# Optimization experiments

Measured on AMD Instinct MI355X. Metric: run time of the kernel, lower is better.

## Reference

```python
import jax, jax.numpy as jnp
import numpy as np

N_NODES = 100000
N_EDGES = 1600000
N_GRAPHS = 512
IN_DIM = 128
HID = 128
N_CLASSES = 10


def _gcn_conv(x, W, b, src, dst, n):
    """PyG GCNConv: out = D^{-1/2} (A+I) D^{-1/2} (x @ W) + b."""
    xw = x @ W  # [n, out_dim]
    loop = jnp.arange(n)
    s = jnp.concatenate([src, loop])  # add self loops
    d = jnp.concatenate([dst, loop])
    deg = jax.ops.segment_sum(jnp.ones(s.shape, dtype=xw.dtype), d, num_segments=n)
    dinv = jnp.where(deg > 0, jax.lax.rsqrt(deg), jnp.zeros((), xw.dtype))
    norm = dinv[s] * dinv[d]  # [E + n]
    out = jax.ops.segment_sum(xw[s] * norm[:, None], d, num_segments=n)
    return out + b


def _global_mean_pool(x, batch, num_graphs):
    sums = jax.ops.segment_sum(x, batch, num_segments=num_graphs)
    cnts = jax.ops.segment_sum(jnp.ones(batch.shape, dtype=x.dtype), batch, num_segments=num_graphs)
    return sums / jnp.maximum(cnts, 1.0)[:, None]


def setup_inputs() -> dict:
    key = jax.random.key(0)
    ks = jax.random.split(key, 8)
    x = jax.random.normal(ks[0], (N_NODES, IN_DIM), dtype=jnp.float32)
    edge_index = jax.random.randint(ks[1], (2, N_EDGES), 0, N_NODES, dtype=jnp.int64)
    batch = jnp.sort(jax.random.randint(ks[2], (N_NODES,), 0, N_GRAPHS, dtype=jnp.int64))
    sc = 1.0 / np.sqrt(IN_DIM)
    W1 = jax.random.normal(ks[3], (IN_DIM, HID), dtype=jnp.float32) * sc
    b1 = jnp.zeros((HID,), dtype=jnp.float32)
    W2 = jax.random.normal(ks[4], (HID, HID), dtype=jnp.float32) * (1.0 / np.sqrt(HID))
    b2 = jnp.zeros((HID,), dtype=jnp.float32)
    Wc = jax.random.normal(ks[5], (HID, N_CLASSES), dtype=jnp.float32) * (1.0 / np.sqrt(HID))
    bc = jnp.zeros((N_CLASSES,), dtype=jnp.float32)
    return {"x": x, "edge_index": edge_index, "batch": batch,
            "W1": W1, "b1": b1, "W2": W2, "b2": b2, "Wc": Wc, "bc": bc}


def reference(x, edge_index, batch, W1, b1, W2, b2, Wc, bc):
    src, dst = edge_index[0], edge_index[1]
    n = x.shape[0]
    h = _gcn_conv(x, W1, b1, src, dst, n)
    h = jax.nn.relu(h)
    h = _gcn_conv(h, W2, b2, src, dst, n)
    g = _global_mean_pool(h, batch, N_GRAPHS)
    return g @ Wc + bc
```

## Files before the change

### kernel.cpp

```cpp
#include <hip/hip_runtime.h>

#define N_NODES 100000
#define N_EDGES 1600000
#define N_GRAPHS 512
#define DIM 128
#define NCLS 10
#define NBKT 782
#define BCAP 2560

typedef __attribute__((ext_vector_type(8))) short short8;
typedef __attribute__((ext_vector_type(4))) float f32x4;

static __device__ __forceinline__ unsigned short f2bf(float f) {
    unsigned u = __float_as_uint(f);
    unsigned r = (u + 0x7FFF + ((u >> 16) & 1)) >> 16;
    return (unsigned short)r;
}
static __device__ __forceinline__ float bf2f(unsigned u) {
    return __uint_as_float(u << 16);
}


__global__ void k_wprep(const float* __restrict__ W1, const float* __restrict__ W2,
                        unsigned short* __restrict__ wf1, unsigned short* __restrict__ wf2,
                        int* __restrict__ bcnt, int* __restrict__ deg) {
    int b = blockIdx.x;
    if (b >= 128) {
        if (b < 132) {
            int i = (b - 128) * 256 + threadIdx.x;
            if (i < NBKT) bcnt[i] = 0;
        } else {
            int i = (b - 132) * 256 + threadIdx.x;
            if (i < N_NODES) deg[i] = 0;
        }
        return;
    }
    const float* W = (b < 64) ? W1 : W2;
    unsigned short* wfrag = (b < 64) ? wf1 : wf2;
    int t = (b & 63) * 256 + threadIdx.x;
    int j = t & 7, lane = (t >> 3) & 63, nt = (t >> 9) & 7, kit = t >> 12;
    int k = kit * 32 + (lane >> 4) * 8 + j;
    int n = nt * 16 + (lane & 15);
    float v = W[k * 128 + n];
    unsigned short h = f2bf(v);
    wfrag[t] = h;
    wfrag[16384 + t] = f2bf(v - bf2f(h));
}


__global__ __launch_bounds__(256) void k_bucket(
    const int* __restrict__ src, const int* __restrict__ dst,
    int* __restrict__ bcnt, unsigned* __restrict__ bpack,
    int* __restrict__ deg, int E) {
    __shared__ int cnt[NBKT];
    __shared__ int base[NBKT];
    int tid = threadIdx.x;
    for (int i = tid; i < NBKT; i += 256) cnt[i] = 0;
    __syncthreads();
    int e0 = blockIdx.x * 4096 + tid;
    unsigned pk[16]; short bk[16];
#pragma unroll
    for (int j = 0; j < 16; j++) {
        int e = e0 + j * 256;
        if (e < E) {
            int s = src[e], d = dst[e];
            atomicAdd(&deg[d], 1);
            bk[j] = (short)(d >> 7);
            pk[j] = ((unsigned)(d & 127) << 17) | (unsigned)s;
            atomicAdd(&cnt[bk[j]], 1);
        } else bk[j] = -1;
    }
    __syncthreads();
    for (int i = tid; i < NBKT; i += 256) {
        int c = cnt[i];
        base[i] = c ? atomicAdd(&bcnt[i], c) : 0;
        cnt[i] = 0;
    }
    __syncthreads();
#pragma unroll
    for (int j = 0; j < 16; j++) {
        if (bk[j] >= 0) {
            int p = base[bk[j]] + atomicAdd(&cnt[bk[j]], 1);
            if (p < BCAP) bpack[(size_t)bk[j] * BCAP + p] = pk[j];
        }
    }
}


static __device__ __forceinline__ void bsort_body(
    char* smemraw, int b,
    const unsigned* __restrict__ bpack, const int* __restrict__ bcnt,
    int* __restrict__ rp, float* __restrict__ dinv,
    int* __restrict__ esrc, int N) {
    int* lds      = (int*)smemraw;
    int* cnt      = lds + 256;
    int* scan     = lds + 384;
    int* cur      = lds + 512;
    int* gbase_sh = lds + 640;
    int tid = threadIdx.x;
    int v[4], pre[4];
    int s = 0;
#pragma unroll
    for (int j = 0; j < 4; j++) {
        int idx = tid * 4 + j;
        v[j] = (idx < NBKT) ? min(bcnt[idx], BCAP) : 0;
        pre[j] = s; s += v[j];
    }
    lds[tid] = s;
    __syncthreads();
    for (int off = 1; off < 256; off <<= 1) {
        int t = (tid >= off) ? lds[tid - off] : 0;
        __syncthreads();
        lds[tid] += t;
        __syncthreads();
    }
    if (tid == (b >> 2)) *gbase_sh = lds[tid] - s + pre[b & 3];
    if (tid < 128) cnt[tid] = 0;
    __syncthreads();
    int gbase = *gbase_sh;
    int n0 = b << 7;
    int m = min(bcnt[b], BCAP);
    const unsigned* bp = bpack + (size_t)b * BCAP;
    for (int j = tid; j < m; j += 256) atomicAdd(&cnt[bp[j] >> 17], 1);
    __syncthreads();
    if (tid < 128) scan[tid] = cnt[tid];
    __syncthreads();
    for (int off = 1; off < 128; off <<= 1) {
        int t = (tid < 128 && tid >= off) ? scan[tid - off] : 0;
        __syncthreads();
        if (tid < 128) scan[tid] += t;
        __syncthreads();
    }
    if (tid < 128) {
        int c = cnt[tid];
        int excl = scan[tid] - c;
        int node = n0 + tid;
        if (node <= N) rp[node] = gbase + excl;
        if (node < N) dinv[node] = rsqrtf((float)(c + 1));
        cur[tid] = gbase + excl;
    }
    __syncthreads();
    for (int j = tid; j < m; j += 256) {
        unsigned pk = bp[j];
        int p = atomicAdd(&cur[pk >> 17], 1);
        esrc[p] = (int)(pk & 0x1FFFF);
    }
}

static __device__ __forceinline__ void gemm_f32_body(
    char* smemraw, int rowBlk,
    const float* __restrict__ A, const unsigned short* __restrict__ wfrag,
    const int* __restrict__ deg, unsigned short* __restrict__ ybf, int M) {
    unsigned short* ldsw = (unsigned short*)smemraw;
    int tid = threadIdx.x, wave = tid >> 6, lane = tid & 63;
    int m = lane & 15, quad = lane >> 4;
    int rowBase = rowBlk * 128 + wave * 32;
    int r0 = rowBase + m, r1 = rowBase + 16 + m;
    for (int i = tid; i < 2048; i += 256)
        ((short8*)ldsw)[i] = ((const short8*)wfrag)[i];
    __syncthreads();
    f32x4 acc0[8], acc1[8];
#pragma unroll
    for (int i = 0; i < 8; i++) { acc0[i] = (f32x4){0,0,0,0}; acc1[i] = (f32x4){0,0,0,0}; }
    const unsigned short* wlo = wfrag + 16384;

#pragma unroll
    for (int kit = 0; kit < 4; kit++) {
        float a0[8], a1[8];
        if (r0 < M) {
            const float4* ap = (const float4*)(A + (size_t)r0 * 128 + kit * 32 + quad * 8);
            float4 f0 = ap[0], f1 = ap[1];
            a0[0]=f0.x; a0[1]=f0.y; a0[2]=f0.z; a0[3]=f0.w; a0[4]=f1.x; a0[5]=f1.y; a0[6]=f1.z; a0[7]=f1.w;
        } else { for (int j = 0; j < 8; j++) a0[j] = 0.f; }
        if (r1 < M) {
            const float4* ap = (const float4*)(A + (size_t)r1 * 128 + kit * 32 + quad * 8);
            float4 f0 = ap[0], f1 = ap[1];
            a1[0]=f0.x; a1[1]=f0.y; a1[2]=f0.z; a1[3]=f0.w; a1[4]=f1.x; a1[5]=f1.y; a1[6]=f1.z; a1[7]=f1.w;
        } else { for (int j = 0; j < 8; j++) a1[j] = 0.f; }
        short8 ahi0, alo0, ahi1, alo1;
#pragma unroll
        for (int j = 0; j < 8; j++) {
            unsigned short h0 = f2bf(a0[j]);
            ahi0[j] = (short)h0; alo0[j] = (short)f2bf(a0[j] - bf2f(h0));
            unsigned short h1 = f2bf(a1[j]);
            ahi1[j] = (short)h1; alo1[j] = (short)f2bf(a1[j] - bf2f(h1));
        }
        int fb = kit * 4096 + lane * 8;
#pragma unroll
        for (int nt = 0; nt < 8; nt++) {
            int idx = fb + nt * 512;
            short8 bhi = *(const short8*)(ldsw + idx);
            short8 blo = *(const short8*)(wlo + idx);
            acc0[nt] = __builtin_amdgcn_mfma_f32_16x16x32_bf16(ahi0, bhi, acc0[nt], 0, 0, 0);
            acc0[nt] = __builtin_amdgcn_mfma_f32_16x16x32_bf16(alo0, bhi, acc0[nt], 0, 0, 0);
            acc0[nt] = __builtin_amdgcn_mfma_f32_16x16x32_bf16(ahi0, blo, acc0[nt], 0, 0, 0);
            acc1[nt] = __builtin_amdgcn_mfma_f32_16x16x32_bf16(ahi1, bhi, acc1[nt], 0, 0, 0);
            acc1[nt] = __builtin_amdgcn_mfma_f32_16x16x32_bf16(alo1, bhi, acc1[nt], 0, 0, 0);
            acc1[nt] = __builtin_amdgcn_mfma_f32_16x16x32_bf16(ahi1, blo, acc1[nt], 0, 0, 0);
        }
    }
    __syncthreads();
    float dv0 = (r0 < M) ? rsqrtf((float)deg[r0] + 1.0f) : 0.f;
    float dv1 = (r1 < M) ? rsqrtf((float)deg[r1] + 1.0f) : 0.f;
    unsigned short* wsm = ldsw + wave * 32 * 136;
#pragma unroll
    for (int rg = 0; rg < 4; rg++) {
        float s0 = __shfl(dv0, quad * 4 + rg);
        float s1 = __shfl(dv1, quad * 4 + rg);
#pragma unroll
        for (int nt = 0; nt < 8; nt++) {
            wsm[(quad * 4 + rg) * 136 + nt * 16 + m] = f2bf(acc0[nt][rg] * s0);
            wsm[(16 + quad * 4 + rg) * 136 + nt * 16 + m] = f2bf(acc1[nt][rg] * s1);
        }
    }
    __syncthreads();
#pragma unroll
    for (int i = 0; i < 8; i++) {
        int rl = i * 4 + quad;
        int grow = rowBase + rl;
        if (grow < M) {
            short8 v = *(const short8*)(wsm + rl * 136 + m * 8);
            *(short8*)(ybf + (size_t)grow * 128 + m * 8) = v;
        }
    }
}


__global__ __launch_bounds__(256) void k_p3(
    const unsigned* __restrict__ bpack, const int* __restrict__ bcnt,
    int* __restrict__ rp, float* __restrict__ dinv, int* __restrict__ esrc, int N,
    const float* __restrict__ A, const unsigned short* __restrict__ wfrag,
    const int* __restrict__ deg, unsigned short* __restrict__ ybf, int M) {
    __shared__ __align__(16) char smem[4 * 32 * 136 * 2];
    if ((int)blockIdx.x < NBKT) bsort_body(smem, blockIdx.x, bpack, bcnt, rp, dinv, esrc, N);
    else                        gemm_f32_body(smem, blockIdx.x - NBKT, A, wfrag, deg, ybf, M);
}


__global__ __launch_bounds__(256) void k_gemm_bf(
    const unsigned short* __restrict__ A, const unsigned short* __restrict__ wfrag,
    const float* __restrict__ dinv, unsigned short* __restrict__ ybf, int M) {
    __shared__ unsigned short ldsw[4 * 32 * 136];
    int tid = threadIdx.x, wave = tid >> 6, lane = tid & 63;
    int m = lane & 15, quad = lane >> 4;
    int rowBase = blockIdx.x * 128 + wave * 32;
    int r0 = rowBase + m, r1 = rowBase + 16 + m;
    for (int i = tid; i < 2048; i += 256)
        ((short8*)ldsw)[i] = ((const short8*)wfrag)[i];
    __syncthreads();
    f32x4 acc0[8], acc1[8];
#pragma unroll
    for (int i = 0; i < 8; i++) { acc0[i] = (f32x4){0,0,0,0}; acc1[i] = (f32x4){0,0,0,0}; }
    const unsigned short* wlo = wfrag + 16384;

#pragma unroll
    for (int kit = 0; kit < 4; kit++) {
        short8 ah0, ah1;
        if (r0 < M) ah0 = *(const short8*)(A + (size_t)r0 * 128 + kit * 32 + quad * 8);
        else { for (int j = 0; j < 8; j++) ah0[j] = 0; }
        if (r1 < M) ah1 = *(const short8*)(A + (size_t)r1 * 128 + kit * 32 + quad * 8);
        else { for (int j = 0; j < 8; j++) ah1[j] = 0; }
        int fb = kit * 4096 + lane * 8;
#pragma unroll
        for (int nt = 0; nt < 8; nt++) {
            int idx = fb + nt * 512;
            short8 bhi = *(const short8*)(ldsw + idx);
            short8 blo = *(const short8*)(wlo + idx);
            acc0[nt] = __builtin_amdgcn_mfma_f32_16x16x32_bf16(ah0, bhi, acc0[nt], 0, 0, 0);
            acc0[nt] = __builtin_amdgcn_mfma_f32_16x16x32_bf16(ah0, blo, acc0[nt], 0, 0, 0);
            acc1[nt] = __builtin_amdgcn_mfma_f32_16x16x32_bf16(ah1, bhi, acc1[nt], 0, 0, 0);
            acc1[nt] = __builtin_amdgcn_mfma_f32_16x16x32_bf16(ah1, blo, acc1[nt], 0, 0, 0);
        }
    }
    __syncthreads();
    float dv0 = (r0 < M) ? dinv[r0] : 0.f;
    float dv1 = (r1 < M) ? dinv[r1] : 0.f;
    unsigned short* wsm = ldsw + wave * 32 * 136;
#pragma unroll
    for (int rg = 0; rg < 4; rg++) {
        float s0 = __shfl(dv0, quad * 4 + rg);
        float s1 = __shfl(dv1, quad * 4 + rg);
#pragma unroll
        for (int nt = 0; nt < 8; nt++) {
            wsm[(quad * 4 + rg) * 136 + nt * 16 + m] = f2bf(acc0[nt][rg] * s0);
            wsm[(16 + quad * 4 + rg) * 136 + nt * 16 + m] = f2bf(acc1[nt][rg] * s1);
        }
    }
    __syncthreads();
#pragma unroll
    for (int i = 0; i < 8; i++) {
        int rl = i * 4 + quad;
        int grow = rowBase + rl;
        if (grow < M) {
            short8 v = *(const short8*)(wsm + rl * 136 + m * 8);
            *(short8*)(ybf + (size_t)grow * 128 + m * 8) = v;
        }
    }
}


__global__ __launch_bounds__(256) void k_agg(
    const unsigned short* __restrict__ y, const float* __restrict__ dinv,
    const int* __restrict__ rp, const int* __restrict__ esrc,
    const float* __restrict__ bias, unsigned* __restrict__ out, int relu, int N) {
    int wave = threadIdx.x >> 6;
    int lane = threadIdx.x & 63;
    int node = blockIdx.x * 4 + wave;
    if (node >= N) return;
    const unsigned* y2 = (const unsigned*)y;
    unsigned vs = y2[(size_t)node * 64 + lane];
    float a0 = bf2f(vs & 0xFFFF), a1 = bf2f(vs >> 16);
    int beg = rp[node], end = rp[node + 1];
    int j = beg;
    while (j < end) {
        int idxv = (j + lane < end) ? esrc[j + lane] : 0;
        int cnt = end - j; if (cnt > 64) cnt = 64;
        int i = 0;
        for (; i + 4 <= cnt; i += 4) {
            int s0 = __shfl(idxv, i + 0);
            int s1 = __shfl(idxv, i + 1);
            int s2 = __shfl(idxv, i + 2);
            int s3 = __shfl(idxv, i + 3);
            unsigned v0 = y2[(size_t)s0 * 64 + lane];
            unsigned v1 = y2[(size_t)s1 * 64 + lane];
            unsigned v2 = y2[(size_t)s2 * 64 + lane];
            unsigned v3 = y2[(size_t)s3 * 64 + lane];
            a0 += bf2f(v0 & 0xFFFF); a1 += bf2f(v0 >> 16);
            a0 += bf2f(v1 & 0xFFFF); a1 += bf2f(v1 >> 16);
            a0 += bf2f(v2 & 0xFFFF); a1 += bf2f(v2 >> 16);
            a0 += bf2f(v3 & 0xFFFF); a1 += bf2f(v3 >> 16);
        }
        for (; i < cnt; i++) {
            int s = __shfl(idxv, i);
            unsigned v = y2[(size_t)s * 64 + lane];
            a0 += bf2f(v & 0xFFFF); a1 += bf2f(v >> 16);
        }
        j += cnt;
    }
    float s = dinv[node];
    float2 bv = ((const float2*)bias)[lane];
    float o0 = s * a0 + bv.x;
    float o1 = s * a1 + bv.y;
    if (relu) { o0 = fmaxf(o0, 0.f); o1 = fmaxf(o1, 0.f); }
    out[(size_t)node * 64 + lane] = (unsigned)f2bf(o0) | ((unsigned)f2bf(o1) << 16);
}


__global__ __launch_bounds__(256) void k_poolhead(
    const unsigned* __restrict__ h2, const int* __restrict__ batch,
    const float* __restrict__ Wc, const float* __restrict__ bc,
    float* __restrict__ out, int n) {
    __shared__ float2 red[4][64];
    __shared__ float grow[DIM];
    int gid = blockIdx.x;
    int tid = threadIdx.x, wave = tid >> 6, lane = tid & 63;
    int lo = 0, hi = n;
    while (lo < hi) { int mid = (lo + hi) >> 1; if (batch[mid] < gid) lo = mid + 1; else hi = mid; }
    int start = lo;
    hi = n;
    while (lo < hi) { int mid = (lo + hi) >> 1; if (batch[mid] < gid + 1) lo = mid + 1; else hi = mid; }
    int end = lo;
    float a0 = 0.f, a1 = 0.f;
    for (int r = start + wave; r < end; r += 4) {
        unsigned v = h2[(size_t)r * 64 + lane];
        a0 += bf2f(v & 0xFFFF); a1 += bf2f(v >> 16);
    }
    red[wave][lane] = make_float2(a0, a1);
    __syncthreads();
    if (tid < 64) {
        float2 s = red[0][tid];
        s.x += red[1][tid].x; s.y += red[1][tid].y;
        s.x += red[2][tid].x; s.y += red[2][tid].y;
        s.x += red[3][tid].x; s.y += red[3][tid].y;
        int cnt = end - start;
        float inv = 1.f / (float)(cnt > 0 ? cnt : 1);
        grow[tid * 2] = s.x * inv;
        grow[tid * 2 + 1] = s.y * inv;
    }
    __syncthreads();
    if (tid < NCLS) {
        float acc = bc[tid];
#pragma unroll 16
        for (int k = 0; k < DIM; k++) acc += grow[k] * Wc[k * NCLS + tid];
        out[gid * NCLS + tid] = acc;
    }
}

extern "C" void kernel_launch(void* const* d_in, const int* in_sizes, int n_in,
                              void* d_out, int out_size, void* d_ws, size_t ws_size,
                              hipStream_t stream) {
    const float* x    = (const float*)d_in[0];
    const int*   ei   = (const int*)d_in[1];
    const int*   batch= (const int*)d_in[2];
    const float* W1   = (const float*)d_in[3];
    const float* b1   = (const float*)d_in[4];
    const float* W2   = (const float*)d_in[5];
    const float* b2   = (const float*)d_in[6];
    const float* Wc   = (const float*)d_in[7];
    const float* bc   = (const float*)d_in[8];
    float* out = (float*)d_out;
    const int N = N_NODES, E = N_EDGES;
    const int* src = ei;
    const int* dst = ei + E;

    char* ws = (char*)d_ws;
    size_t off = 0;
    auto carve = [&](size_t bytes) -> void* {
        void* p = ws + off;
        off = (off + bytes + 255) & ~(size_t)255;
        return p;
    };
    int*      rp    = (int*)     carve((size_t)(N + 1) * 4);
    float*    dinv  = (float*)   carve((size_t)N * 4);
    int*      bcnt  = (int*)     carve(NBKT * 4);
    int*      deg   = (int*)     carve((size_t)N * 4);
    unsigned* bpack = (unsigned*)carve((size_t)NBKT * BCAP * 4);
    int*      esrc  = (int*)     carve((size_t)E * 4);
    unsigned short* wf1 = (unsigned short*)carve(2 * 16384 * 2);
    unsigned short* wf2 = (unsigned short*)carve(2 * 16384 * 2);
    unsigned short* bufY = (unsigned short*)carve((size_t)N * DIM * 2);
    unsigned short* bufH = (unsigned short*)carve((size_t)N * DIM * 2);
    (void)ws_size; (void)n_in; (void)in_sizes; (void)out_size;

    const int nbBkt = (E + 4095) / 4096;
    const int gemmGrid = (N + 127) / 128;
    const int degZero = (N + 255) / 256;

    hipLaunchKernelGGL(k_wprep, dim3(132 + degZero), dim3(256), 0, stream, W1, W2, wf1, wf2, bcnt, deg);
    hipLaunchKernelGGL(k_bucket, dim3(nbBkt), dim3(256), 0, stream, src, dst, bcnt, bpack, deg, E);
    hipLaunchKernelGGL(k_p3, dim3(NBKT + gemmGrid), dim3(256), 0, stream,
                       bpack, bcnt, rp, dinv, esrc, N, x, wf1, deg, bufY, N);
    hipLaunchKernelGGL(k_agg, dim3((N + 3) / 4), dim3(256), 0, stream, bufY, dinv, rp, esrc, b1, (unsigned*)bufH, 1, N);
    hipLaunchKernelGGL(k_gemm_bf, dim3(gemmGrid), dim3(256), 0, stream, bufH, wf2, dinv, bufY, N);
    hipLaunchKernelGGL(k_agg, dim3((N + 3) / 4), dim3(256), 0, stream, bufY, dinv, rp, esrc, b2, (unsigned*)bufH, 0, N);
    hipLaunchKernelGGL(k_poolhead, dim3(N_GRAPHS), dim3(256), 0, stream, (const unsigned*)bufH, batch, Wc, bc, out, N);
}
```

Baseline: 386.4 us.

## Fuse bucket sort with first GEMM per block and drop global degree atomics

Removes the global per-edge degree atomics and the deg array. Degrees now come from the per-bucket counts computed during the bucket sort. Each block of the merged kernel sorts one 128-node bucket, keeps the normalisation factors in shared memory, then runs the first-layer GEMM for the same 128 rows. This drops 1.6M global atomics and the zeroing pass, but the sort and GEMM phases within a block now run in sequence, no longer as separate concurrent blocks.

```diff
diff --git a/kernel.cpp b/kernel.cpp
--- a/kernel.cpp
+++ b/kernel.cpp
@@ -23,16 +23,11 @@
 
 __global__ void k_wprep(const float* __restrict__ W1, const float* __restrict__ W2,
                         unsigned short* __restrict__ wf1, unsigned short* __restrict__ wf2,
-                        int* __restrict__ bcnt, int* __restrict__ deg) {
+                        int* __restrict__ bcnt) {
     int b = blockIdx.x;
     if (b >= 128) {
-        if (b < 132) {
-            int i = (b - 128) * 256 + threadIdx.x;
-            if (i < NBKT) bcnt[i] = 0;
-        } else {
-            int i = (b - 132) * 256 + threadIdx.x;
-            if (i < N_NODES) deg[i] = 0;
-        }
+        int i = (b - 128) * 256 + threadIdx.x;
+        if (i < NBKT) bcnt[i] = 0;
         return;
     }
     const float* W = (b < 64) ? W1 : W2;
@@ -50,8 +45,7 @@
 
 __global__ __launch_bounds__(256) void k_bucket(
     const int* __restrict__ src, const int* __restrict__ dst,
-    int* __restrict__ bcnt, unsigned* __restrict__ bpack,
-    int* __restrict__ deg, int E) {
+    int* __restrict__ bcnt, unsigned* __restrict__ bpack, int E) {
     __shared__ int cnt[NBKT];
     __shared__ int base[NBKT];
     int tid = threadIdx.x;
@@ -64,7 +58,6 @@
         int e = e0 + j * 256;
         if (e < E) {
             int s = src[e], d = dst[e];
-            atomicAdd(&deg[d], 1);
             bk[j] = (short)(d >> 7);
             pk[j] = ((unsigned)(d & 127) << 17) | (unsigned)s;
             atomicAdd(&cnt[bk[j]], 1);
@@ -91,7 +84,7 @@
     char* smemraw, int b,
     const unsigned* __restrict__ bpack, const int* __restrict__ bcnt,
     int* __restrict__ rp, float* __restrict__ dinv,
-    int* __restrict__ esrc, int N) {
+    int* __restrict__ esrc, int N, float* __restrict__ dvs) {
     int* lds      = (int*)smemraw;
     int* cnt      = lds + 256;
     int* scan     = lds + 384;
@@ -135,8 +128,10 @@
         int c = cnt[tid];
         int excl = scan[tid] - c;
         int node = n0 + tid;
+        float dv = rsqrtf((float)(c + 1));
         if (node <= N) rp[node] = gbase + excl;
-        if (node < N) dinv[node] = rsqrtf((float)(c + 1));
+        if (node < N) dinv[node] = dv;
+        dvs[tid] = dv;
         cur[tid] = gbase + excl;
     }
     __syncthreads();
@@ -150,7 +145,7 @@
 static __device__ __forceinline__ void gemm_f32_body(
     char* smemraw, int rowBlk,
     const float* __restrict__ A, const unsigned short* __restrict__ wfrag,
-    const int* __restrict__ deg, unsigned short* __restrict__ ybf, int M) {
+    const float* __restrict__ dvs, unsigned short* __restrict__ ybf, int M) {
     unsigned short* ldsw = (unsigned short*)smemraw;
     int tid = threadIdx.x, wave = tid >> 6, lane = tid & 63;
     int m = lane & 15, quad = lane >> 4;
@@ -200,13 +195,11 @@
         }
     }
     __syncthreads();
-    float dv0 = (r0 < M) ? rsqrtf((float)deg[r0] + 1.0f) : 0.f;
-    float dv1 = (r1 < M) ? rsqrtf((float)deg[r1] + 1.0f) : 0.f;
     unsigned short* wsm = ldsw + wave * 32 * 136;
 #pragma unroll
     for (int rg = 0; rg < 4; rg++) {
-        float s0 = __shfl(dv0, quad * 4 + rg);
-        float s1 = __shfl(dv1, quad * 4 + rg);
+        float s0 = dvs[wave * 32 + quad * 4 + rg];
+        float s1 = dvs[wave * 32 + 16 + quad * 4 + rg];
 #pragma unroll
         for (int nt = 0; nt < 8; nt++) {
             wsm[(quad * 4 + rg) * 136 + nt * 16 + m] = f2bf(acc0[nt][rg] * s0);
@@ -226,14 +219,17 @@
 }
 
 
-__global__ __launch_bounds__(256) void k_p3(
+__global__ __launch_bounds__(256) void k_fuse(
     const unsigned* __restrict__ bpack, const int* __restrict__ bcnt,
     int* __restrict__ rp, float* __restrict__ dinv, int* __restrict__ esrc, int N,
     const float* __restrict__ A, const unsigned short* __restrict__ wfrag,
-    const int* __restrict__ deg, unsigned short* __restrict__ ybf, int M) {
+    unsigned short* __restrict__ ybf, int M) {
     __shared__ __align__(16) char smem[4 * 32 * 136 * 2];
-    if ((int)blockIdx.x < NBKT) bsort_body(smem, blockIdx.x, bpack, bcnt, rp, dinv, esrc, N);
-    else                        gemm_f32_body(smem, blockIdx.x - NBKT, A, wfrag, deg, ybf, M);
+    __shared__ float dvs[128];
+    int b = blockIdx.x;
+    bsort_body(smem, b, bpack, bcnt, rp, dinv, esrc, N, dvs);
+    __syncthreads();
+    gemm_f32_body(smem, b, A, wfrag, dvs, ybf, M);
 }
 
 
@@ -413,7 +409,6 @@
     int*      rp    = (int*)     carve((size_t)(N + 1) * 4);
     float*    dinv  = (float*)   carve((size_t)N * 4);
     int*      bcnt  = (int*)     carve(NBKT * 4);
-    int*      deg   = (int*)     carve((size_t)N * 4);
     unsigned* bpack = (unsigned*)carve((size_t)NBKT * BCAP * 4);
     int*      esrc  = (int*)     carve((size_t)E * 4);
     unsigned short* wf1 = (unsigned short*)carve(2 * 16384 * 2);
@@ -424,12 +419,11 @@
 
     const int nbBkt = (E + 4095) / 4096;
     const int gemmGrid = (N + 127) / 128;
-    const int degZero = (N + 255) / 256;
-
-    hipLaunchKernelGGL(k_wprep, dim3(132 + degZero), dim3(256), 0, stream, W1, W2, wf1, wf2, bcnt, deg);
-    hipLaunchKernelGGL(k_bucket, dim3(nbBkt), dim3(256), 0, stream, src, dst, bcnt, bpack, deg, E);
-    hipLaunchKernelGGL(k_p3, dim3(NBKT + gemmGrid), dim3(256), 0, stream,
-                       bpack, bcnt, rp, dinv, esrc, N, x, wf1, deg, bufY, N);
+
+    hipLaunchKernelGGL(k_wprep,  dim3(128 + (NBKT + 255) / 256), dim3(256), 0, stream, W1, W2, wf1, wf2, bcnt);
+    hipLaunchKernelGGL(k_bucket, dim3(nbBkt), dim3(256), 0, stream, src, dst, bcnt, bpack, E);
+    hipLaunchKernelGGL(k_fuse, dim3(NBKT), dim3(256), 0, stream,
+                       bpack, bcnt, rp, dinv, esrc, N, x, wf1, bufY, N);
     hipLaunchKernelGGL(k_agg, dim3((N + 3) / 4), dim3(256), 0, stream, bufY, dinv, rp, esrc, b1, (unsigned*)bufH, 1, N);
     hipLaunchKernelGGL(k_gemm_bf, dim3(gemmGrid), dim3(256), 0, stream, bufH, wf2, dinv, bufY, N);
     hipLaunchKernelGGL(k_agg, dim3((N + 3) / 4), dim3(256), 0, stream, bufY, dinv, rp, esrc, b2, (unsigned*)bufH, 0, N);
```

Result: faster. 337.7 us (-12.6%).
